# Optimization experiments

Hardware: AMD Instinct MI355X
Metric: run time of the kernel (lower is better)

## Reference

```python
import jax, jax.numpy as jnp
import numpy as np
import math

B = 50        # graphs per batch
NPG = 2000    # nodes per graph
EPG = 12000   # edges per graph
F_IN = 256
NHID = 128
RATIO = 0.8


def setup_inputs() -> dict:
    key = jax.random.key(0)
    ks = jax.random.split(key, 12)
    N = B * NPG
    src_loc = jax.random.randint(ks[0], (B, EPG), 0, NPG)
    dst_loc = jax.random.randint(ks[1], (B, EPG), 0, NPG)
    off = (jnp.arange(B) * NPG)[:, None]
    edge_index = jnp.stack([(src_loc + off).reshape(-1), (dst_loc + off).reshape(-1)]).astype(jnp.int32)

    def lin(k, fi, fo):
        return (jax.random.normal(k, (fi, fo), jnp.float32) / np.sqrt(fi).astype(np.float32))

    return {
        "x": jax.random.normal(ks[2], (N, F_IN), jnp.float32),
        "W1": lin(ks[3], F_IN, NHID), "b1": jnp.zeros(NHID, jnp.float32),
        "Ws1": lin(ks[4], NHID, 1), "bs1": jnp.zeros(1, jnp.float32),
        "W2": lin(ks[5], NHID, NHID), "b2": jnp.zeros(NHID, jnp.float32),
        "Ws2": lin(ks[6], NHID, 1), "bs2": jnp.zeros(1, jnp.float32),
        "W3": lin(ks[7], NHID, NHID), "b3": jnp.zeros(NHID, jnp.float32),
        "Ws3": lin(ks[8], NHID, 1), "bs3": jnp.zeros(1, jnp.float32),
        "Wl": lin(ks[9], 2 * NHID, NHID), "bl": jnp.zeros(NHID, jnp.float32),
        "edge_index": edge_index,
    }


def gcn_conv(x, W, b, src, dst, w, N):
    # PyG GCNConv: D^{-1/2} (A + I) D^{-1/2} X W + b, deg from edge weights + self loop
    h = x @ W
    deg = jax.ops.segment_sum(w, dst, num_segments=N) + 1.0
    dis = jax.lax.rsqrt(deg)
    norm = w * dis[src] * dis[dst]                       # [E]
    agg = jax.ops.segment_sum(h[src] * norm[:, None], dst, num_segments=N)
    return agg + h / deg[:, None] + b                    # self-loop norm = 1/deg


def sag_pool(x, src, dst, w, Ws, bs, n_per_graph):
    N = x.shape[0]
    k = math.ceil(RATIO * n_per_graph)
    score = gcn_conv(x, Ws, bs, src, dst, w, N)[:, 0]    # [N]
    _, topi = jax.lax.top_k(score.reshape(B, n_per_graph), k)
    perm = (topi + (jnp.arange(B) * n_per_graph)[:, None]).reshape(-1)
    x_new = x[perm] * jnp.tanh(score[perm])[:, None]
    # filter_adj: keep edges whose endpoints survive, reindex; dropped edges -> weight 0
    mapping = jnp.full((N,), -1, jnp.int32).at[perm].set(jnp.arange(B * k, dtype=jnp.int32))
    ns, nd = mapping[src], mapping[dst]
    valid = (ns >= 0) & (nd >= 0) & (w > 0)
    return (x_new, jnp.where(valid, ns, 0), jnp.where(valid, nd, 0),
            jnp.where(valid, w, jnp.zeros((), x.dtype)), k)


def readout(x, n):
    # global max pool || global mean pool (equal-size graphs, nodes grouped per graph)
    xr = x.reshape(B, n, -1)
    return jnp.concatenate([xr.max(axis=1), xr.mean(axis=1)], axis=-1)


def reference(x, W1, b1, Ws1, bs1, W2, b2, Ws2, bs2, W3, b3, Ws3, bs3, Wl, bl, edge_index):
    src, dst = edge_index[0], edge_index[1]
    w = jnp.ones(src.shape[0], x.dtype)
    n = NPG
    x = jax.nn.relu(gcn_conv(x, W1, b1, src, dst, w, B * n))
    x, src, dst, w, n = sag_pool(x, src, dst, w, Ws1, bs1, n)
    x1 = readout(x, n)
    x = jax.nn.relu(gcn_conv(x, W2, b2, src, dst, w, B * n))
    x, src, dst, w, n = sag_pool(x, src, dst, w, Ws2, bs2, n)
    x2 = readout(x, n)
    x = jax.nn.relu(gcn_conv(x, W3, b3, src, dst, w, B * n))
    x, src, dst, w, n = sag_pool(x, src, dst, w, Ws3, bs3, n)
    x3 = readout(x, n)
    return jax.nn.relu((x1 + x2 + x3) @ Wl + bl)
```

## Files before the change

kernel.cpp:

```cpp
#include <hip/hip_runtime.h>
#include <math.h>

#define B_GRAPHS 50
#define NPG0     2000
#define EPG      12000
#define F_IN_C   256
#define NHID     128
#define N0       (B_GRAPHS * NPG0)
#define NE       (B_GRAPHS * EPG)
#define RSEG     32
#define GSLOTS   7
#define CPAD     136
#define KMAX     1600

typedef _Float16 f16x8 __attribute__((ext_vector_type(8)));
typedef float    f32x4 __attribute__((ext_vector_type(4)));

static inline int cdiv(int a, int b) { return (a + b - 1) / b; }

__global__ void k_fill_start(int* __restrict__ cnt, float* __restrict__ accum) {
    int i = blockIdx.x * 256 + threadIdx.x;
    if (i < N0) cnt[i] = 0;
    if (i < B_GRAPHS * 256) accum[i] = 0.f;
}

__global__ void k_init_cvt(const int* __restrict__ ei, int* __restrict__ esrc,
                           int* __restrict__ edst, float* __restrict__ ew,
                           int* __restrict__ cnt,
                           const float* __restrict__ W1, const float* __restrict__ W2,
                           const float* __restrict__ W3, _Float16* __restrict__ WT1,
                           _Float16* __restrict__ WT2, _Float16* __restrict__ WT3) {
    int t = blockIdx.x * 256 + threadIdx.x;
    if (t < NE) {
        int d = ei[NE + t];
        esrc[t] = ei[t]; edst[t] = d; ew[t] = 1.0f;
        atomicAdd(&cnt[d], 1);
    }
    if (t < 128 * 256) {
        int n = t >> 8, kk = t & 255;
        WT1[t] = (_Float16)W1[kk * 128 + n];
    } else if (t < 128 * 256 + 128 * 128) {
        int u = t - 32768; int n = u >> 7, kk = u & 127;
        WT2[u] = (_Float16)W2[kk * 128 + n];
    } else if (t < 128 * 256 + 2 * 128 * 128) {
        int u = t - 49152; int n = u >> 7, kk = u & 127;
        WT3[u] = (_Float16)W3[kk * 128 + n];
    }
}

template<int FP32IN, int F, int GATHER, int POOL>
__global__ __launch_bounds__(256) void k_gemm_ws(const void* __restrict__ Xin,
                                                 const _Float16* __restrict__ WT,
                                                 const int* __restrict__ perm,
                                                 const float* __restrict__ gate,
                                                 _Float16* __restrict__ H, int N,
                                                 float* __restrict__ pmax,
                                                 float* __restrict__ psum) {
    constexpr int KH  = (F > 128) ? 128 : F;
    constexpr int K8H = KH / 8;
    constexpr int SMEMSZ = (128 * KH > 64 * CPAD) ? 128 * KH : 64 * CPAD;
    __shared__ _Float16 smem[SMEMSZ];
    const int tid  = threadIdx.x;
    const int wave = tid >> 6, lane = tid & 63;
    const int quad = lane >> 4, l16 = lane & 15;
    const int m_blk = blockIdx.x * 64;

    f32x4 acc[8];
#pragma unroll
    for (int j = 0; j < 8; ++j) acc[j] = {0.f, 0.f, 0.f, 0.f};

    int row0 = m_blk + wave * 16 + l16;
    if (row0 > N - 1) row0 = N - 1;
    _Float16 g0 = (_Float16)1.0f;
    float g0f = 1.0f;
    if (GATHER) {
        g0f = gate[row0];
        g0 = (_Float16)g0f;
        row0 = perm[row0];
    }
    const int sx = l16 & 7;
    constexpr int NKQ = F / 32;

    f16x8 q0[NKQ];

    if (FP32IN) {
        constexpr int PD = (NKQ < 4) ? NKQ : 4;
        const float* base0 = (const float*)Xin + (size_t)row0 * F + quad * 8;
        float4 p0[PD][2];
#pragma unroll
        for (int i = 0; i < PD; ++i) {
            p0[i][0] = ((const float4*)(base0 + i * 32))[0];
            p0[i][1] = ((const float4*)(base0 + i * 32))[1];
        }
#pragma unroll
        for (int c = tid; c < 128 * K8H; c += 256) {
            int n = c / K8H, k8 = c - n * K8H;
            f16x8 v = *(const f16x8*)&WT[(size_t)(n * (F / 8) + k8) * 8];
            *(f16x8*)&smem[n * KH + ((k8 ^ (n & 7)) << 3)] = v;
        }
        __syncthreads();
#pragma unroll
        for (int kq = 0; kq < NKQ; ++kq) {
            if (KH < F && kq == NKQ / 2) {
                __syncthreads();
#pragma unroll
                for (int c = tid; c < 128 * K8H; c += 256) {
                    int n = c / K8H, k8 = c - n * K8H;
                    f16x8 v = *(const f16x8*)&WT[(size_t)(n * (F / 8) + K8H + k8) * 8];
                    *(f16x8*)&smem[n * KH + ((k8 ^ (n & 7)) << 3)] = v;
                }
                __syncthreads();
            }
            const int b = kq % PD;
            float4 f0 = p0[b][0], f1 = p0[b][1];
            if (kq + PD < NKQ) {
                p0[b][0] = ((const float4*)(base0 + (kq + PD) * 32))[0];
                p0[b][1] = ((const float4*)(base0 + (kq + PD) * 32))[1];
            }
            f16x8 af0 = (f16x8){(_Float16)f0.x,(_Float16)f0.y,(_Float16)f0.z,(_Float16)f0.w,
                                (_Float16)f1.x,(_Float16)f1.y,(_Float16)f1.z,(_Float16)f1.w};
            f16x8 bf[8];
#pragma unroll
            for (int j = 0; j < 8; ++j)
                bf[j] = *(const f16x8*)&smem[(j * 16 + l16) * KH + (((((kq & 3) << 2) + quad) ^ sx) << 3)];
#pragma unroll
            for (int j = 0; j < 8; ++j)
                acc[j] = __builtin_amdgcn_mfma_f32_16x16x32_f16(af0, bf[j], acc[j], 0, 0, 0);
        }
    } else {
#pragma unroll
        for (int c = tid; c < 128 * K8H; c += 256) {
            int n = c / K8H, k8 = c - n * K8H;
            f16x8 v = *(const f16x8*)&WT[(size_t)(n * K8H + k8) * 8];
            *(f16x8*)&smem[n * KH + ((k8 ^ (n & 7)) << 3)] = v;
        }
        const _Float16* base0 = (const _Float16*)Xin + (size_t)row0 * F + quad * 8;
#pragma unroll
        for (int i = 0; i < NKQ; ++i)
            q0[i] = *(const f16x8*)(base0 + i * 32);
        __syncthreads();
#pragma unroll
        for (int kq = 0; kq < NKQ; ++kq) {
            f16x8 af0 = q0[kq];
            if (GATHER) af0 = af0 * g0;
            f16x8 bf[8];
#pragma unroll
            for (int j = 0; j < 8; ++j)
                bf[j] = *(const f16x8*)&smem[(j * 16 + l16) * KH + (((((kq & 3) << 2) + quad) ^ sx) << 3)];
#pragma unroll
            for (int j = 0; j < 8; ++j)
                acc[j] = __builtin_amdgcn_mfma_f32_16x16x32_f16(af0, bf[j], acc[j], 0, 0, 0);
        }
    }
    __syncthreads();

    _Float16* sC = smem;
    const int rw = wave * 16;
#pragma unroll
    for (int j = 0; j < 8; ++j)
#pragma unroll
        for (int g = 0; g < 4; ++g)
            sC[(rw + quad * 4 + g) * CPAD + j * 16 + l16] = (_Float16)acc[j][g];
    __syncthreads();
    {
        int rr = tid >> 2;
        int cc = (tid & 3) * 32;
        int gr = m_blk + rr;
        if (gr < N) {
            _Float16* Hr = H + (size_t)gr * 128 + cc;
            const _Float16* Sr = sC + rr * CPAD + cc;
#pragma unroll
            for (int c = 0; c < 4; ++c)
                *(f16x8*)&Hr[c * 8] = *(const f16x8*)&Sr[c * 8];
        }
    }
    if (POOL && GATHER && !FP32IN) {
        __syncthreads();
        float* smax = (float*)smem;
        float* ssum = smax + 4 * 128;
#pragma unroll
        for (int kq = 0; kq < NKQ; ++kq) {
#pragma unroll
            for (int j = 0; j < 8; ++j) {
                float v = (float)q0[kq][j] * g0f;
                float mx = v, sm = v;
#pragma unroll
                for (int s2 = 1; s2 < 16; s2 <<= 1) {
                    mx = fmaxf(mx, __shfl_xor(mx, s2, 64));
                    sm += __shfl_xor(sm, s2, 64);
                }
                if (l16 == 0) {
                    int f = kq * 32 + quad * 8 + j;
                    smax[wave * 128 + f] = mx;
                    ssum[wave * 128 + f] = sm;
                }
            }
        }
        __syncthreads();
        if (tid < 128) {
            float mx = fmaxf(fmaxf(smax[tid], smax[128 + tid]),
                             fmaxf(smax[256 + tid], smax[384 + tid]));
            float sm = ssum[tid] + ssum[128 + tid] + ssum[256 + tid] + ssum[384 + tid];
            int kprev = N / B_GRAPHS;
            int g = m_blk / kprev;
            int blkg = (m_blk - g * kprev) >> 6;
            pmax[(size_t)(g * RSEG + blkg) * NHID + tid] = mx;
            psum[(size_t)(g * RSEG + blkg) * NHID + tid] = sm;
        }
    }
}

__global__ __launch_bounds__(1024) void k_scancsr(const int* __restrict__ cnt,
                                                  int* __restrict__ offs,
                                                  const int* __restrict__ esrc,
                                                  const int* __restrict__ edst,
                                                  const float* __restrict__ ew,
                                                  int* __restrict__ csr_src,
                                                  float* __restrict__ csr_norm,
                                                  int npg) {
    __shared__ int ch[1024];
    __shared__ int scnt[2048];
    __shared__ int scur[2048];
    int b = blockIdx.x, tid = threadIdx.x;
    int base = b * npg;
    int per = (npg + 1023) >> 10;
    int s0 = tid * per;
    int s1 = s0 + per; if (s1 > npg) s1 = npg; if (s0 > npg) s0 = npg;
    int s = 0;
    for (int i = s0; i < s1; ++i) { int c = cnt[base + i]; scnt[i] = c; s += c; }
    ch[tid] = s;
    __syncthreads();
    for (int d = 1; d < 1024; d <<= 1) {
        int t = ch[tid] + ((tid >= d) ? ch[tid - d] : 0);
        __syncthreads();
        ch[tid] = t;
        __syncthreads();
    }
    int run = b * EPG + ch[tid] - s;
    for (int i = s0; i < s1; ++i) {
        offs[base + i] = run; scur[i] = run;
        run += scnt[i];
    }
    __syncthreads();
    int e0 = b * EPG;
    for (int e = tid; e < EPG; e += 1024) {
        float w = ew[e0 + e];
        if (w > 0.f) {
            int sN = esrc[e0 + e], d = edst[e0 + e];
            int pos = atomicAdd(&scur[d - base], 1);
            csr_src[pos] = sN;
            csr_norm[pos] = rsqrtf((float)(scnt[sN - base] + 1)) *
                            rsqrtf((float)(scnt[d - base] + 1));
        }
    }
}

__global__ __launch_bounds__(256) void k_agg(const _Float16* __restrict__ H,
                                             const int* __restrict__ csr_src,
                                             const float* __restrict__ csr_norm,
                                             const int* __restrict__ offs,
                                             const int* __restrict__ cnt,
                                             const float* __restrict__ bias,
                                             const float* __restrict__ Ws,
                                             _Float16* __restrict__ X,
                                             float* __restrict__ hs,
                                             int bpg, int npg) {
    int bi = blockIdx.x;
    int x = bi & 7, s = bi >> 3;
    int gslot = s / bpg, blk = s - gslot * bpg;
    int g = x + 8 * gslot;
    if (g >= B_GRAPHS) return;
    int node = g * npg + blk * 4 + (threadIdx.x >> 6);
    int lane = threadIdx.x & 63;
    int quad = lane >> 4, l16 = lane & 15;

    int st = offs[node], c = cnt[node], en = st + c;
    float acc[8];
#pragma unroll
    for (int j = 0; j < 8; ++j) acc[j] = 0.f;

    if (c > 0) {
        for (int e0 = st; e0 < en; e0 += 8) {
            int eA = e0 + quad, eB = eA + 4;
            int ecA = eA < en ? eA : en - 1;
            int ecB = eB < en ? eB : en - 1;
            int uA = csr_src[ecA], uB = csr_src[ecB];
            float nA = (eA < en) ? csr_norm[ecA] : 0.f;
            float nB = (eB < en) ? csr_norm[ecB] : 0.f;
            f16x8 hA = *(const f16x8*)&H[(size_t)uA * NHID + l16 * 8];
            f16x8 hB = *(const f16x8*)&H[(size_t)uB * NHID + l16 * 8];
#pragma unroll
            for (int j = 0; j < 8; ++j) acc[j] = fmaf((float)hA[j], nA, acc[j]);
#pragma unroll
            for (int j = 0; j < 8; ++j) acc[j] = fmaf((float)hB[j], nB, acc[j]);
        }
    }
#pragma unroll
    for (int j = 0; j < 8; ++j) {
        acc[j] += __shfl_xor(acc[j], 16, 64);
        acc[j] += __shfl_xor(acc[j], 32, 64);
    }
    float invd = 1.f / (float)(c + 1);
    f16x8 hn = *(const f16x8*)&H[(size_t)node * NHID + l16 * 8];
    float4 b0 = *(const float4*)&bias[l16 * 8];
    float4 b1 = *(const float4*)&bias[l16 * 8 + 4];
    float4 w0 = *(const float4*)&Ws[l16 * 8];
    float4 w1 = *(const float4*)&Ws[l16 * 8 + 4];
    const float bb[8] = {b0.x, b0.y, b0.z, b0.w, b1.x, b1.y, b1.z, b1.w};
    const float ww[8] = {w0.x, w0.y, w0.z, w0.w, w1.x, w1.y, w1.z, w1.w};
    float sd = 0.f;
    f16x8 o;
#pragma unroll
    for (int j = 0; j < 8; ++j) {
        float v = fmaxf(acc[j] + (float)hn[j] * invd + bb[j], 0.f);
        o[j] = (_Float16)v;
        sd = fmaf(v, ww[j], sd);
    }
    if (quad == 0)
        *(f16x8*)&X[(size_t)node * NHID + l16 * 8] = o;
    sd += __shfl_xor(sd, 1, 64);
    sd += __shfl_xor(sd, 2, 64);
    sd += __shfl_xor(sd, 4, 64);
    sd += __shfl_xor(sd, 8, 64);
    if (lane == 0) hs[node] = sd;
}

template<int REMAP, int COMB>
__global__ __launch_bounds__(1024) void k_scoretopk(const float* __restrict__ hs,
                                                    int* __restrict__ csr_src,
                                                    float* __restrict__ csr_norm,
                                                    int* __restrict__ offs,
                                                    const int* __restrict__ cnt,
                                                    const float* __restrict__ bs,
                                                    int* __restrict__ perm,
                                                    float* __restrict__ gate,
                                                    int* __restrict__ esrc,
                                                    int* __restrict__ edst,
                                                    float* __restrict__ ew,
                                                    int* __restrict__ cntN,
                                                    const float* __restrict__ pmax,
                                                    const float* __restrict__ psum,
                                                    float* __restrict__ accum,
                                                    int npg, int k, int nseg) {
    __shared__ float ss[2048];
    __shared__ int   si[2048];
    __shared__ float shs[2048];
    __shared__ int   shist[KMAX];
    int b = blockIdx.x, tid = threadIdx.x;
    int base = b * npg;

    if (COMB) {
        if (tid < 2 * NHID) {
            int f = tid & 127;
            bool isSum = tid >= NHID;
            float a2 = isSum ? 0.f : -__builtin_inff();
            for (int s = 0; s < nseg; ++s) {
                float v = (isSum ? psum : pmax)[(size_t)(b * RSEG + s) * NHID + f];
                a2 = isSum ? (a2 + v) : fmaxf(a2, v);
            }
            if (isSum) accum[b * 256 + 128 + f] += a2 / (float)npg;
            else       accum[b * 256 + f]       += a2;
        }
    }

    float bs0 = bs[0];
    for (int i = tid; i < 2048; i += 1024)
        shs[i] = (i < npg) ? hs[base + i] : 0.f;
    __syncthreads();
    for (int i = tid; i < 2048; i += 1024) {
        if (i < npg) {
            int st = offs[base + i], c = cnt[base + i];
            float a = 0.f;
            for (int e = st; e < st + c; ++e)
                a = fmaf(shs[csr_src[e] - base], csr_norm[e], a);
            ss[i] = a + shs[i] / (float)(c + 1) + bs0;
        } else {
            ss[i] = -__builtin_inff();
        }
        si[i] = i;
    }
    __syncthreads();

    const int wbase = (tid >> 6) << 7;
    const int l = tid & 63;
    float vL = ss[wbase + l],      vH = ss[wbase + 64 + l];
    int   iL = si[wbase + l],      iH = si[wbase + 64 + l];

    auto reg_steps = [&](int size, int smax) {
        for (int s = smax; s > 0; s >>= 1) {
            if (s == 64) {
                bool fwd = (((wbase + l) & size) == 0);
                bool bba = (vH > vL) || (vH == vL && iH < iL);
                if (fwd ? bba : !bba) {
                    float tv = vL; vL = vH; vH = tv;
                    int ti = iL; iL = iH; iH = ti;
                }
            } else {
                bool iR = ((l & s) == 0);
                float pv = __shfl_xor(vL, s, 64);
                int   pi = __shfl_xor(iL, s, 64);
                float sa = iR ? vL : pv, sb = iR ? pv : vL;
                int   ia = iR ? iL : pi, ib = iR ? pi : iL;
                bool bba = (sb > sa) || (sb == sa && ib < ia);
                bool fwd = (((wbase + l) & size) == 0);
                if (fwd ? bba : !bba) { vL = pv; iL = pi; }
                pv = __shfl_xor(vH, s, 64);
                pi = __shfl_xor(iH, s, 64);
                sa = iR ? vH : pv; sb = iR ? pv : vH;
                ia = iR ? iH : pi; ib = iR ? pi : iH;
                bba = (sb > sa) || (sb == sa && ib < ia);
                bool fwd2 = (((wbase + 64 + l) & size) == 0);
                if (fwd2 ? bba : !bba) { vH = pv; iH = pi; }
            }
        }
    };

    for (int size = 2; size <= 128; size <<= 1)
        reg_steps(size, size >> 1);
    for (int size = 256; size <= 2048; size <<= 1) {
        ss[wbase + l] = vL;      si[wbase + l] = iL;
        ss[wbase + 64 + l] = vH; si[wbase + 64 + l] = iH;
        __syncthreads();
        for (int stride = size >> 1; stride >= 128; stride >>= 1) {
            int i = ((tid & ~(stride - 1)) << 1) | (tid & (stride - 1));
            int j = i | stride;
            float sa = ss[i], sb = ss[j];
            int   ia = si[i], ib = si[j];
            bool bba = (sb > sa) || (sb == sa && ib < ia);
            bool fwd = ((i & size) == 0);
            if (fwd ? bba : !bba) { ss[i] = sb; ss[j] = sa; si[i] = ib; si[j] = ia; }
            __syncthreads();
        }
        vL = ss[wbase + l];      iL = si[wbase + l];
        vH = ss[wbase + 64 + l]; iH = si[wbase + 64 + l];
        reg_steps(size, 64);
    }
    ss[wbase + l] = vL;      si[wbase + l] = iL;
    ss[wbase + 64 + l] = vH; si[wbase + 64 + l] = iH;
    __syncthreads();

    int* smap = (int*)shs;
    for (int j = tid; j < npg; j += 1024) {
        int ol = si[j];
        if (j < k) {
            int newg = b * k + j;
            perm[newg] = base + ol;
            smap[ol] = newg;
            gate[newg] = tanhf(ss[j]);
        } else {
            smap[ol] = -1;
        }
    }
    if (REMAP) {
        for (int j = tid; j < k; j += 1024) shist[j] = 0;
        __syncthreads();
        int e0 = b * EPG;
        for (int e = tid; e < EPG; e += 1024) {
            int idx = e0 + e;
            float w = ew[idx];
            bool valid = false;
            int ns = 0, nd = 0;
            if (w > 0.f) {
                ns = smap[esrc[idx] - base];
                nd = smap[edst[idx] - base];
                valid = (ns >= 0) && (nd >= 0);
            }
            esrc[idx] = valid ? ns : 0;
            edst[idx] = valid ? nd : 0;
            ew[idx]   = valid ? w : 0.f;
            if (valid) atomicAdd(&shist[nd - b * k], 1);
        }
        __syncthreads();
        int* sscan = (int*)ss;
        int* scur  = si;
        int per2 = (k + 1023) >> 10;
        int t0 = tid * per2, t1 = t0 + per2;
        if (t1 > k) t1 = k; if (t0 > k) t0 = k;
        int sloc = 0;
        for (int i = t0; i < t1; ++i) sloc += shist[i];
        sscan[tid] = sloc;
        __syncthreads();
        for (int d = 1; d < 1024; d <<= 1) {
            int t = sscan[tid] + ((tid >= d) ? sscan[tid - d] : 0);
            __syncthreads();
            sscan[tid] = t;
            __syncthreads();
        }
        int run = b * EPG + sscan[tid] - sloc;
        for (int i = t0; i < t1; ++i) {
            offs[b * k + i] = run; scur[i] = run;
            cntN[b * k + i] = shist[i];
            run += shist[i];
        }
        __syncthreads();
        for (int e = tid; e < EPG; e += 1024) {
            int idx = e0 + e;
            float w = ew[idx];
            if (w > 0.f) {
                int ns = esrc[idx], nd = edst[idx];
                int pos = atomicAdd(&scur[nd - b * k], 1);
                csr_src[pos] = ns;
                csr_norm[pos] = rsqrtf((float)(shist[ns - b * k] + 1)) *
                                rsqrtf((float)(shist[nd - b * k] + 1));
            }
        }
    }
}

__global__ __launch_bounds__(128) void k_pool_readout(const _Float16* __restrict__ X,
                                                      const float* __restrict__ gate,
                                                      const int* __restrict__ perm,
                                                      float* __restrict__ pmax,
                                                      float* __restrict__ psum, int k) {
    int s = blockIdx.x, b = blockIdx.y, f = threadIdx.x;
    int j0 = (k * s) / RSEG, j1 = (k * (s + 1)) / RSEG;
    float mx = -__builtin_inff(), sm = 0.f;
    for (int j = j0; j < j1; ++j) {
        int g = b * k + j;
        int old = perm[g];
        float v = (float)X[(size_t)old * NHID + f] * gate[g];
        mx = fmaxf(mx, v);
        sm += v;
    }
    pmax[(size_t)(b * RSEG + s) * NHID + f] = mx;
    psum[(size_t)(b * RSEG + s) * NHID + f] = sm;
}

__global__ __launch_bounds__(128) void k_comb_final(const float* __restrict__ pmax,
                                                    const float* __restrict__ psum,
                                                    const float* __restrict__ accum,
                                                    const float* __restrict__ Wl,
                                                    const float* __restrict__ bl,
                                                    float* __restrict__ out, int k) {
    __shared__ float a[256];
    int b = blockIdx.x, f = threadIdx.x;
    float mx = -__builtin_inff(), sm = 0.f;
#pragma unroll
    for (int s = 0; s < RSEG; ++s) {
        mx = fmaxf(mx, pmax[(size_t)(b * RSEG + s) * NHID + f]);
        sm += psum[(size_t)(b * RSEG + s) * NHID + f];
    }
    a[f]       = accum[b * 256 + f] + mx;
    a[128 + f] = accum[b * 256 + 128 + f] + sm / (float)k;
    __syncthreads();
    float s = bl[f];
    for (int i = 0; i < 256; ++i) s = fmaf(a[i], Wl[i * NHID + f], s);
    out[b * NHID + f] = fmaxf(s, 0.f);
}

extern "C" void kernel_launch(void* const* d_in, const int* in_sizes, int n_in,
                              void* d_out, int out_size, void* d_ws, size_t ws_size,
                              hipStream_t stream) {
    const float* x0 = (const float*)d_in[0];
    const float* Wm[3] = {(const float*)d_in[1], (const float*)d_in[5], (const float*)d_in[9]};
    const float* bm[3] = {(const float*)d_in[2], (const float*)d_in[6], (const float*)d_in[10]};
    const float* Wsc[3] = {(const float*)d_in[3], (const float*)d_in[7], (const float*)d_in[11]};
    const float* bsc[3] = {(const float*)d_in[4], (const float*)d_in[8], (const float*)d_in[12]};
    const float* Wl = (const float*)d_in[13];
    const float* bl = (const float*)d_in[14];
    const int*   ei = (const int*)d_in[15];
    float* out = (float*)d_out;

    _Float16* bufA = (_Float16*)d_ws;
    _Float16* bufB = bufA + (size_t)N0 * NHID;
    _Float16* WT1  = bufB + (size_t)N0 * NHID;
    _Float16* WT2  = WT1 + 128 * 256;
    _Float16* WT3  = WT2 + 128 * 128;
    float* hs     = (float*)(WT3 + 128 * 128);
    float* gate   = hs + N0;
    float* accum  = gate + N0;
    float* pmax   = accum + B_GRAPHS * 256;
    float* psum   = pmax + B_GRAPHS * RSEG * NHID;
    int*   cntA   = (int*)(psum + B_GRAPHS * RSEG * NHID);
    int*   cntB   = cntA + N0;
    int*   offs   = cntB + N0;
    int*   perm   = offs + N0;
    int*   esrc   = perm + N0;
    int*   edst   = esrc + NE;
    float* ew     = (float*)(edst + NE);
    int*   csr_src= (int*)(ew + NE);
    float* csr_norm = (float*)(csr_src + NE);

    _Float16* WTs[3] = {WT1, WT2, WT3};
    const int EG = cdiv(NE, 256);

    k_fill_start<<<cdiv(N0, 256), 256, 0, stream>>>(cntA, accum);
    k_init_cvt<<<EG, 256, 0, stream>>>(ei, esrc, edst, ew, cntA,
                                       Wm[0], Wm[1], Wm[2], WT1, WT2, WT3);

    int npg = NPG0;
    _Float16* Hbuf = bufA; _Float16* Xbuf = bufB;

    for (int layer = 0; layer < 3; ++layer) {
        int N = B_GRAPHS * npg;
        int k = (npg * 4) / 5;
        int bpg = npg >> 2;
        int* cnt  = (layer == 1) ? cntB : cntA;
        int* cntN = (layer == 1) ? cntA : cntB;
        int nseg = npg >> 6;

        if (layer == 0) {
            k_gemm_ws<1, 256, 0, 0><<<cdiv(N, 64), 256, 0, stream>>>(
                x0, WTs[0], perm, gate, Hbuf, N, pmax, psum);
            k_scancsr<<<B_GRAPHS, 1024, 0, stream>>>(cnt, offs, esrc, edst, ew,
                                                     csr_src, csr_norm, npg);
        } else {
            k_gemm_ws<0, 128, 1, 1><<<cdiv(N, 64), 256, 0, stream>>>(
                Xbuf, WTs[layer], perm, gate, Hbuf, N, pmax, psum);
        }
        k_agg<<<8 * GSLOTS * bpg, 256, 0, stream>>>(Hbuf, csr_src, csr_norm, offs, cnt,
                                                    bm[layer], Wsc[layer], Xbuf, hs, bpg, npg);
        if (layer == 0)
            k_scoretopk<1, 0><<<B_GRAPHS, 1024, 0, stream>>>(hs, csr_src, csr_norm, offs, cnt,
                                                             bsc[layer], perm, gate,
                                                             esrc, edst, ew, cntN,
                                                             pmax, psum, accum, npg, k, 0);
        else if (layer == 1)
            k_scoretopk<1, 1><<<B_GRAPHS, 1024, 0, stream>>>(hs, csr_src, csr_norm, offs, cnt,
                                                             bsc[layer], perm, gate,
                                                             esrc, edst, ew, cntN,
                                                             pmax, psum, accum, npg, k, nseg);
        else
            k_scoretopk<0, 1><<<B_GRAPHS, 1024, 0, stream>>>(hs, csr_src, csr_norm, offs, cnt,
                                                             bsc[layer], perm, gate,
                                                             esrc, edst, ew, cntN,
                                                             pmax, psum, accum, npg, k, nseg);
        if (layer == 2) {
            k_pool_readout<<<dim3(RSEG, B_GRAPHS), 128, 0, stream>>>(Xbuf, gate, perm,
                                                                     pmax, psum, k);
            k_comb_final<<<B_GRAPHS, 128, 0, stream>>>(pmax, psum, accum, Wl, bl, out, k);
        }

        npg = k;
    }
}
```

Before: 539.2 us.

## Fuse edge init, degree count and CSR build into one per-graph kernel

Replaces the fill, edge-convert and scan/CSR kernels with one kernel that has one block per graph. Each block counts in-degrees with shared-memory atomics, scans, and builds the CSR, while extra blocks convert the weights to fp16. It also drops accum zeroing by having the first readout combine store rather than accumulate. This removes two launches and the global atomics and count round-trip, but only 114 blocks run the setup phase.

```diff
diff --git a/kernel.cpp b/kernel.cpp
--- a/kernel.cpp
+++ b/kernel.cpp
@@ -18,33 +18,74 @@
 
 static inline int cdiv(int a, int b) { return (a + b - 1) / b; }
 
-__global__ void k_fill_start(int* __restrict__ cnt, float* __restrict__ accum) {
-    int i = blockIdx.x * 256 + threadIdx.x;
-    if (i < N0) cnt[i] = 0;
-    if (i < B_GRAPHS * 256) accum[i] = 0.f;
-}
-
-__global__ void k_init_cvt(const int* __restrict__ ei, int* __restrict__ esrc,
-                           int* __restrict__ edst, float* __restrict__ ew,
-                           int* __restrict__ cnt,
-                           const float* __restrict__ W1, const float* __restrict__ W2,
-                           const float* __restrict__ W3, _Float16* __restrict__ WT1,
-                           _Float16* __restrict__ WT2, _Float16* __restrict__ WT3) {
-    int t = blockIdx.x * 256 + threadIdx.x;
-    if (t < NE) {
-        int d = ei[NE + t];
-        esrc[t] = ei[t]; edst[t] = d; ew[t] = 1.0f;
-        atomicAdd(&cnt[d], 1);
-    }
-    if (t < 128 * 256) {
-        int n = t >> 8, kk = t & 255;
-        WT1[t] = (_Float16)W1[kk * 128 + n];
-    } else if (t < 128 * 256 + 128 * 128) {
-        int u = t - 32768; int n = u >> 7, kk = u & 127;
-        WT2[u] = (_Float16)W2[kk * 128 + n];
-    } else if (t < 128 * 256 + 2 * 128 * 128) {
-        int u = t - 49152; int n = u >> 7, kk = u & 127;
-        WT3[u] = (_Float16)W3[kk * 128 + n];
+__global__ __launch_bounds__(1024) void k_csr_init(const int* __restrict__ ei,
+                                                   int* __restrict__ esrc,
+                                                   int* __restrict__ edst,
+                                                   float* __restrict__ ew,
+                                                   int* __restrict__ cnt,
+                                                   int* __restrict__ offs,
+                                                   int* __restrict__ csr_src,
+                                                   float* __restrict__ csr_norm,
+                                                   const float* __restrict__ W1,
+                                                   const float* __restrict__ W2,
+                                                   const float* __restrict__ W3,
+                                                   _Float16* __restrict__ WT1,
+                                                   _Float16* __restrict__ WT2,
+                                                   _Float16* __restrict__ WT3,
+                                                   int npg) {
+    __shared__ int ch[1024];
+    __shared__ int scnt[2048];
+    __shared__ int scur[2048];
+    int bid = blockIdx.x, tid = threadIdx.x;
+    if (bid >= B_GRAPHS) {
+        int t = (bid - B_GRAPHS) * 1024 + tid;
+        if (t < 128 * 256) {
+            int n = t >> 8, kk = t & 255;
+            WT1[t] = (_Float16)W1[kk * 128 + n];
+        } else if (t < 128 * 256 + 128 * 128) {
+            int u = t - 32768; int n = u >> 7, kk = u & 127;
+            WT2[u] = (_Float16)W2[kk * 128 + n];
+        } else if (t < 128 * 256 + 2 * 128 * 128) {
+            int u = t - 49152; int n = u >> 7, kk = u & 127;
+            WT3[u] = (_Float16)W3[kk * 128 + n];
+        }
+        return;
+    }
+    int b = bid, base = b * npg, e0 = b * EPG;
+    for (int i = tid; i < npg; i += 1024) scnt[i] = 0;
+    __syncthreads();
+    for (int e = tid; e < EPG; e += 1024) {
+        int s = ei[e0 + e], d = ei[NE + e0 + e];
+        esrc[e0 + e] = s; edst[e0 + e] = d; ew[e0 + e] = 1.0f;
+        atomicAdd(&scnt[d - base], 1);
+    }
+    __syncthreads();
+    int per = (npg + 1023) >> 10;
+    int s0 = tid * per;
+    int s1 = s0 + per; if (s1 > npg) s1 = npg; if (s0 > npg) s0 = npg;
+    int s = 0;
+    for (int i = s0; i < s1; ++i) s += scnt[i];
+    ch[tid] = s;
+    __syncthreads();
+    for (int d = 1; d < 1024; d <<= 1) {
+        int t = ch[tid] + ((tid >= d) ? ch[tid - d] : 0);
+        __syncthreads();
+        ch[tid] = t;
+        __syncthreads();
+    }
+    int run = e0 + ch[tid] - s;
+    for (int i = s0; i < s1; ++i) {
+        cnt[base + i] = scnt[i];
+        offs[base + i] = run; scur[i] = run;
+        run += scnt[i];
+    }
+    __syncthreads();
+    for (int e = tid; e < EPG; e += 1024) {
+        int sN = esrc[e0 + e], d = edst[e0 + e];
+        int pos = atomicAdd(&scur[d - base], 1);
+        csr_src[pos] = sN;
+        csr_norm[pos] = rsqrtf((float)(scnt[sN - base] + 1)) *
+                        rsqrtf((float)(scnt[d - base] + 1));
     }
 }
 
@@ -206,51 +247,6 @@
             int blkg = (m_blk - g * kprev) >> 6;
             pmax[(size_t)(g * RSEG + blkg) * NHID + tid] = mx;
             psum[(size_t)(g * RSEG + blkg) * NHID + tid] = sm;
-        }
-    }
-}
-
-__global__ __launch_bounds__(1024) void k_scancsr(const int* __restrict__ cnt,
-                                                  int* __restrict__ offs,
-                                                  const int* __restrict__ esrc,
-                                                  const int* __restrict__ edst,
-                                                  const float* __restrict__ ew,
-                                                  int* __restrict__ csr_src,
-                                                  float* __restrict__ csr_norm,
-                                                  int npg) {
-    __shared__ int ch[1024];
-    __shared__ int scnt[2048];
-    __shared__ int scur[2048];
-    int b = blockIdx.x, tid = threadIdx.x;
-    int base = b * npg;
-    int per = (npg + 1023) >> 10;
-    int s0 = tid * per;
-    int s1 = s0 + per; if (s1 > npg) s1 = npg; if (s0 > npg) s0 = npg;
-    int s = 0;
-    for (int i = s0; i < s1; ++i) { int c = cnt[base + i]; scnt[i] = c; s += c; }
-    ch[tid] = s;
-    __syncthreads();
-    for (int d = 1; d < 1024; d <<= 1) {
-        int t = ch[tid] + ((tid >= d) ? ch[tid - d] : 0);
-        __syncthreads();
-        ch[tid] = t;
-        __syncthreads();
-    }
-    int run = b * EPG + ch[tid] - s;
-    for (int i = s0; i < s1; ++i) {
-        offs[base + i] = run; scur[i] = run;
-        run += scnt[i];
-    }
-    __syncthreads();
-    int e0 = b * EPG;
-    for (int e = tid; e < EPG; e += 1024) {
-        float w = ew[e0 + e];
-        if (w > 0.f) {
-            int sN = esrc[e0 + e], d = edst[e0 + e];
-            int pos = atomicAdd(&scur[d - base], 1);
-            csr_src[pos] = sN;
-            csr_norm[pos] = rsqrtf((float)(scnt[sN - base] + 1)) *
-                            rsqrtf((float)(scnt[d - base] + 1));
         }
     }
 }
@@ -358,8 +354,10 @@
                 float v = (isSum ? psum : pmax)[(size_t)(b * RSEG + s) * NHID + f];
                 a2 = isSum ? (a2 + v) : fmaxf(a2, v);
             }
-            if (isSum) accum[b * 256 + 128 + f] += a2 / (float)npg;
-            else       accum[b * 256 + f]       += a2;
+            float val = isSum ? (a2 / (float)npg) : a2;
+            int idx = b * 256 + (isSum ? 128 + f : f);
+            if (COMB == 2) accum[idx] = val;
+            else           accum[idx] += val;
         }
     }
 
@@ -582,14 +580,14 @@
     float* csr_norm = (float*)(csr_src + NE);
 
     _Float16* WTs[3] = {WT1, WT2, WT3};
-    const int EG = cdiv(NE, 256);
-
-    k_fill_start<<<cdiv(N0, 256), 256, 0, stream>>>(cntA, accum);
-    k_init_cvt<<<EG, 256, 0, stream>>>(ei, esrc, edst, ew, cntA,
-                                       Wm[0], Wm[1], Wm[2], WT1, WT2, WT3);
 
     int npg = NPG0;
     _Float16* Hbuf = bufA; _Float16* Xbuf = bufB;
+
+    k_csr_init<<<B_GRAPHS + 64, 1024, 0, stream>>>(ei, esrc, edst, ew, cntA, offs,
+                                                   csr_src, csr_norm,
+                                                   Wm[0], Wm[1], Wm[2],
+                                                   WT1, WT2, WT3, npg);
 
     for (int layer = 0; layer < 3; ++layer) {
         int N = B_GRAPHS * npg;
@@ -602,8 +600,6 @@
         if (layer == 0) {
             k_gemm_ws<1, 256, 0, 0><<<cdiv(N, 64), 256, 0, stream>>>(
                 x0, WTs[0], perm, gate, Hbuf, N, pmax, psum);
-            k_scancsr<<<B_GRAPHS, 1024, 0, stream>>>(cnt, offs, esrc, edst, ew,
-                                                     csr_src, csr_norm, npg);
         } else {
             k_gemm_ws<0, 128, 1, 1><<<cdiv(N, 64), 256, 0, stream>>>(
                 Xbuf, WTs[layer], perm, gate, Hbuf, N, pmax, psum);
@@ -616,7 +612,7 @@
                                                              esrc, edst, ew, cntN,
                                                              pmax, psum, accum, npg, k, 0);
         else if (layer == 1)
-            k_scoretopk<1, 1><<<B_GRAPHS, 1024, 0, stream>>>(hs, csr_src, csr_norm, offs, cnt,
+            k_scoretopk<1, 2><<<B_GRAPHS, 1024, 0, stream>>>(hs, csr_src, csr_norm, offs, cnt,
                                                              bsc[layer], perm, gate,
                                                              esrc, edst, ew, cntN,
                                                              pmax, psum, accum, npg, k, nseg);
```

Result: no change. 532.3 us (-1.3%).
